# Kernel tuning notes

Measured on AMD Instinct MI355X. Metric: run time of the kernel, lower is better.

The kernel has to match this reference:

```python
import jax, jax.numpy as jnp
import numpy as np

N, E, D = 50000, 800000, 128
SLOPE = 0.2


def setup_inputs() -> dict:
    key = jax.random.key(0)
    ks = jax.random.split(key, 8)
    x = jax.random.normal(ks[0], (N, D), dtype=jnp.float32)
    alpha = jax.random.normal(ks[1], (E, D), dtype=jnp.float32)
    Wl = jax.random.normal(ks[2], (D, D), dtype=jnp.float32) / np.sqrt(D).astype(np.float32)
    bl = jax.random.normal(ks[3], (D,), dtype=jnp.float32) * 0.01
    Wr = jax.random.normal(ks[4], (D, D), dtype=jnp.float32) / np.sqrt(D).astype(np.float32)
    br = jax.random.normal(ks[5], (D,), dtype=jnp.float32) * 0.01
    src = jax.random.randint(ks[6], (E,), 0, N, dtype=jnp.int64)
    dst = jax.random.randint(ks[7], (E,), 0, N, dtype=jnp.int64)
    return {"x": x, "alpha": alpha, "Wl": Wl, "bl": bl, "Wr": Wr, "br": br, "src": src, "dst": dst}


def reference(x, alpha, Wl, bl, Wr, br, src, dst):
    n_nodes = x.shape[0]
    # Dense projections: Mu_l(x), Mu_r(x)  -> [N, D]
    hl = x @ Wl.T + bl
    hr = x @ Wr.T + br
    # Edge-wise score: leakyrelu((h_l[src] + h_r[dst]) * alpha)  -> [E, D]
    s = (jnp.take(hl, src, axis=0) + jnp.take(hr, dst, axis=0)) * alpha
    s = jnp.where(s >= 0, s, SLOPE * s)
    # Edge softmax grouped by destination node (per feature channel), numerically stable
    smax = jax.ops.segment_max(s, dst, num_segments=n_nodes)  # [N, D]
    e = jnp.exp(s - jnp.take(smax, dst, axis=0))
    denom = jax.ops.segment_sum(e, dst, num_segments=n_nodes)  # [N, D]
    att = e / jnp.take(denom, dst, axis=0)
    # Weighted scatter-sum aggregation: sum_{e: dst(e)=v} x[src(e)] * att[e]
    msg = jnp.take(x, src, axis=0) * att  # [E, D]
    return jax.ops.segment_sum(msg, dst, num_segments=n_nodes)  # [N, D]
```

## Files before the change

kernel.cpp:

```cpp
#include <hip/hip_runtime.h>
#include <hip/hip_bf16.h>

#define D 128
#define SLOPE 0.2f
#define CAP 64

typedef float f4 __attribute__((ext_vector_type(4)));
typedef unsigned int v4u __attribute__((ext_vector_type(4)));
typedef unsigned short v4h __attribute__((ext_vector_type(4)));
typedef unsigned int u32;
typedef unsigned short u16;


__global__ void zero_kernel(int* __restrict__ p, int n) {
  int i = blockIdx.x * blockDim.x + threadIdx.x;
  if (i < n) p[i] = 0;
}


__global__ void scatter_bucket(const int* __restrict__ dst, const int* __restrict__ src,
                               int* __restrict__ cnt, long long* __restrict__ eperm, int E) {
  int i = blockIdx.x * blockDim.x + threadIdx.x;
  if (i < E) {
    int d = dst[i];
    int p = atomicAdd(&cnt[d], 1);
    if (p < CAP) {
      long long v = (long long)(unsigned int)i | ((long long)src[i] << 32);
      __builtin_nontemporal_store(v, &eperm[(size_t)d * CAP + p]);
    }
  }
}


__global__ void transpose_w(const float* __restrict__ Wl, const float* __restrict__ Wr,
                            float* __restrict__ wcatT) {
  int i = blockIdx.x * blockDim.x + threadIdx.x;
  int k = i >> 8, c = i & 255;
  float v = (c < D) ? Wl[c * D + k] : Wr[(c - D) * D + k];
  wcatT[k * 256 + c] = v;
}


__device__ __forceinline__ u16 bf16r(float f) {
  u32 u = __float_as_uint(f);
  return (u16)((u + 0x7FFFu + ((u >> 16) & 1u)) >> 16);
}

__global__ __launch_bounds__(256) void gemm_hlr(const float* __restrict__ x,
    const float* __restrict__ wcatT, const float* __restrict__ bl,
    const float* __restrict__ br, u16* __restrict__ hx, float* __restrict__ hr,
    int nrows) {
  __shared__ float xs[64 * 128];
  int t = threadIdx.x;
  int row0 = blockIdx.x << 6;
#pragma unroll
  for (int i = 0; i < 8; ++i) {
    int g = t + (i << 8);
    int r = g >> 5, c4 = (g & 31) << 2;
    int gr = row0 + r;
    float4 v = make_float4(0.f, 0.f, 0.f, 0.f);
    if (gr < nrows) v = *(const float4*)(x + (size_t)gr * D + c4);
    *(float4*)(xs + r * 128 + c4) = v;
  }
  __syncthreads();
  int rg = t >> 5, cg = t & 31;
  int r0 = rg << 3, c0 = cg << 3;
  float acc[8][8];
#pragma unroll
  for (int i = 0; i < 8; ++i)
#pragma unroll
    for (int j = 0; j < 8; ++j) acc[i][j] = 0.f;

  for (int kk = 0; kk < 128; kk += 4) {
    float4 xv[8];
#pragma unroll
    for (int i = 0; i < 8; ++i) xv[i] = *(const float4*)(xs + (r0 + i) * 128 + kk);
#pragma unroll
    for (int dk = 0; dk < 4; ++dk) {
      float4 wa = *(const float4*)(wcatT + (kk + dk) * 256 + c0);
      float4 wb = *(const float4*)(wcatT + (kk + dk) * 256 + c0 + 4);
      float wv0 = wa.x, wv1 = wa.y, wv2 = wa.z, wv3 = wa.w;
      float wv4 = wb.x, wv5 = wb.y, wv6 = wb.z, wv7 = wb.w;
#pragma unroll
      for (int i = 0; i < 8; ++i) {
        float xk = (dk == 0) ? xv[i].x : (dk == 1) ? xv[i].y : (dk == 2) ? xv[i].z : xv[i].w;
        acc[i][0] = fmaf(xk, wv0, acc[i][0]);
        acc[i][1] = fmaf(xk, wv1, acc[i][1]);
        acc[i][2] = fmaf(xk, wv2, acc[i][2]);
        acc[i][3] = fmaf(xk, wv3, acc[i][3]);
        acc[i][4] = fmaf(xk, wv4, acc[i][4]);
        acc[i][5] = fmaf(xk, wv5, acc[i][5]);
        acc[i][6] = fmaf(xk, wv6, acc[i][6]);
        acc[i][7] = fmaf(xk, wv7, acc[i][7]);
      }
    }
  }
  float bias[8];
#pragma unroll
  for (int j = 0; j < 8; ++j) bias[j] = (c0 < D) ? bl[c0 + j] : br[c0 - D + j];
#pragma unroll
  for (int i = 0; i < 8; ++i) {
    int gr = row0 + r0 + i;
    if (gr >= nrows) continue;
    if (c0 < D) {
      v4h a, b2;
#pragma unroll
      for (int j = 0; j < 4; ++j) a[j] = bf16r(acc[i][j] + bias[j]);
#pragma unroll
      for (int j = 0; j < 4; ++j) b2[j] = bf16r(acc[i][4 + j] + bias[4 + j]);
      u16* rowp = hx + (size_t)gr * 256;
      *(v4h*)(rowp + 2 * c0) = a;
      *(v4h*)(rowp + 2 * c0 + 8) = b2;
    } else {
      float* base = hr + (size_t)gr * D + (c0 - D);
      float4 o0 = make_float4(acc[i][0] + bias[0], acc[i][1] + bias[1],
                              acc[i][2] + bias[2], acc[i][3] + bias[3]);
      float4 o1 = make_float4(acc[i][4] + bias[4], acc[i][5] + bias[5],
                              acc[i][6] + bias[6], acc[i][7] + bias[7]);
      *(float4*)(base) = o0;
      *(float4*)(base + 4) = o1;
    }
  }
#pragma unroll
  for (int i = 0; i < 8; ++i) {
    int g = t + (i << 8);
    int r = g >> 5, c4 = (g & 31) << 2;
    int gr = row0 + r;
    if (gr < nrows) {
      const float* sp = xs + r * 128 + c4;
      v4h h;
#pragma unroll
      for (int j = 0; j < 4; ++j) h[j] = bf16r(sp[j]);
      *(v4h*)(hx + (size_t)gr * 256 + 2 * c4 + 4) = h;
    }
  }
}


__device__ __forceinline__ f4 ld4(const float* p) { return *(const f4*)p; }
__device__ __forceinline__ f4 ld4nt(const float* p) {
  return __builtin_nontemporal_load((const f4*)p);
}

__global__ __launch_bounds__(256) void node_attn(const u16* __restrict__ hx,
    const float* __restrict__ alpha, const float* __restrict__ hr,
    const long long* __restrict__ eperm, const int* __restrict__ cnt,
    float* __restrict__ out, int n) {
  int wid = threadIdx.x >> 6, lane = threadIdx.x & 63;
  int v = (blockIdx.x << 2) + wid;
  if (v >= n) return;
  int deg = cnt[v];
  if (deg > CAP) deg = CAP;
  int half = lane >> 5;
  int ch = (lane & 31) << 2;

  if (deg == 0) {
    if (half == 0) {
      f4 z = {0.f, 0.f, 0.f, 0.f};
      *(f4*)(out + (size_t)v * D + ch) = z;
    }
    return;
  }

  const long long* ep = eperm + (size_t)v * CAP;
  f4 hrv = ld4(hr + (size_t)v * D + ch);
  f4 dx = {0.f, 0.f, 0.f, 0.f};
  f4 ox = {0.f, 0.f, 0.f, 0.f};

  int ed[4], ss[4];
  float mk[4];
#define LOADIDX(base, EDA, SSA, MKA)                    \
  {                                                     \
    _Pragma("unroll")                                   \
    for (int u = 0; u < 4; ++u) {                       \
      int idx = (base) + 2 * u + half;                  \
      int j = (idx < deg) ? idx : (deg - 1);            \
      long long pq = ep[j];                             \
      EDA[u] = (int)(unsigned int)pq;                   \
      SSA[u] = (int)(pq >> 32);                         \
      MKA[u] = (idx < deg) ? 1.f : 0.f;                 \
    }                                                   \
  }

  int i = 0;
  LOADIDX(i, ed, ss, mk)
  while (true) {
    f4 av[4];
    v4u gv[4];
#pragma unroll
    for (int u = 0; u < 4; ++u) av[u] = ld4nt(alpha + (size_t)ed[u] * D + ch);
#pragma unroll
    for (int u = 0; u < 4; ++u)
      gv[u] = *(const v4u*)(hx + (size_t)ss[u] * 256 + (ch << 1));

    int inext = i + 8;
    bool more = inext < deg;
    int edn[4], ssn[4];
    float mkn[4];
    if (more) LOADIDX(inext, edn, ssn, mkn)

#pragma unroll
    for (int u = 0; u < 4; ++u) {
      f4 h, xv;
      h[0] = __uint_as_float((gv[u].x & 0xFFFFu) << 16);
      h[1] = __uint_as_float(gv[u].x & 0xFFFF0000u);
      h[2] = __uint_as_float((gv[u].y & 0xFFFFu) << 16);
      h[3] = __uint_as_float(gv[u].y & 0xFFFF0000u);
      xv[0] = __uint_as_float((gv[u].z & 0xFFFFu) << 16);
      xv[1] = __uint_as_float(gv[u].z & 0xFFFF0000u);
      xv[2] = __uint_as_float((gv[u].w & 0xFFFFu) << 16);
      xv[3] = __uint_as_float(gv[u].w & 0xFFFF0000u);
      f4 t = (h + hrv) * av[u];
      f4 ev;
#pragma unroll
      for (int k = 0; k < 4; ++k) {
        float tt = t[k];
        tt = (tt >= 0.f) ? tt : SLOPE * tt;
        ev[k] = __expf(tt);
      }
      ev *= mk[u];
      dx += ev;
      ox += xv * ev;
    }
    if (!more) break;
    i = inext;
#pragma unroll
    for (int u = 0; u < 4; ++u) { ed[u] = edn[u]; ss[u] = ssn[u]; mk[u] = mkn[u]; }
  }
#undef LOADIDX

#pragma unroll
  for (int k = 0; k < 4; ++k) {
    dx[k] += __shfl_xor(dx[k], 32);
    ox[k] += __shfl_xor(ox[k], 32);
  }
  if (half == 0) {
    f4 r;
#pragma unroll
    for (int k = 0; k < 4; ++k) r[k] = ox[k] / dx[k];
    *(f4*)(out + (size_t)v * D + ch) = r;
  }
}

extern "C" void kernel_launch(void* const* d_in, const int* in_sizes, int n_in,
                              void* d_out, int out_size, void* d_ws, size_t ws_size,
                              hipStream_t stream) {
  const float* x = (const float*)d_in[0];
  const float* alpha = (const float*)d_in[1];
  const float* Wl = (const float*)d_in[2];
  const float* bl = (const float*)d_in[3];
  const float* Wr = (const float*)d_in[4];
  const float* br = (const float*)d_in[5];
  const int* src = (const int*)d_in[6];
  const int* dst = (const int*)d_in[7];
  int N = in_sizes[0] / D;
  int E = in_sizes[6];
  float* out = (float*)d_out;

  char* ws = (char*)d_ws;
  auto al = [](size_t v) { return (v + 255) & ~(size_t)255; };
  size_t off = 0;
  u16* hx = (u16*)(ws + off); off += al((size_t)N * 256 * 2);
  float* hr = (float*)(ws + off); off += al((size_t)N * D * 4);
  float* wcatT = (float*)(ws + off); off += al(128 * 256 * 4);
  int* cnt = (int*)(ws + off); off += al((size_t)N * 4);
  long long* eperm = (long long*)(ws + off); off += al((size_t)N * CAP * 8);
  (void)off; (void)ws_size; (void)n_in; (void)out_size;

  const int tb = 256;
  zero_kernel<<<(N + tb - 1) / tb, tb, 0, stream>>>(cnt, N);
  scatter_bucket<<<(E + tb - 1) / tb, tb, 0, stream>>>(dst, src, cnt, eperm, E);
  transpose_w<<<(128 * 256) / tb, tb, 0, stream>>>(Wl, Wr, wcatT);
  gemm_hlr<<<(N + 63) / 64, 256, 0, stream>>>(x, wcatT, bl, br, hx, hr, N);
  node_attn<<<(N + 3) / 4, 256, 0, stream>>>(hx, alpha, hr, eperm, cnt, out, N);
}
```

Measured before the change: 249.5 us.

## Replace FP32 SIMT projection GEMM with bf16 MFMA and pre-converted operands

Adds a pass that converts x to bf16 (also writing the bf16 x half of hx and zeroing counts) and packs the weights into a k-blocked bf16 layout. The scalar-FMA fp32 GEMM is replaced by an MFMA 16x16x32 bf16 kernel where each wave computes 16 rows by 256 columns. The aim is to cut GEMM compute time using matrix cores. In exchange it adds an extra pass over x, lowers projection precision to bf16 inputs, and uses scattered 2-byte output stores.

```diff
diff --git a/kernel.cpp b/kernel.cpp
--- a/kernel.cpp
+++ b/kernel.cpp
@@ -8,13 +8,42 @@
 typedef float f4 __attribute__((ext_vector_type(4)));
 typedef unsigned int v4u __attribute__((ext_vector_type(4)));
 typedef unsigned short v4h __attribute__((ext_vector_type(4)));
+typedef short s8v __attribute__((ext_vector_type(8)));
 typedef unsigned int u32;
 typedef unsigned short u16;
 
-
-__global__ void zero_kernel(int* __restrict__ p, int n) {
+__device__ __forceinline__ u16 bf16r(float f) {
+  u32 u = __float_as_uint(f);
+  return (u16)((u + 0x7FFFu + ((u >> 16) & 1u)) >> 16);
+}
+
+
+__global__ void convert_x(const float* __restrict__ x, u16* __restrict__ xbf,
+                          u16* __restrict__ hx, int* __restrict__ cnt, int N) {
   int i = blockIdx.x * blockDim.x + threadIdx.x;
-  if (i < n) p[i] = 0;
+  if (i < N) cnt[i] = 0;
+  if (i >= N * 16) return;
+  int row = i >> 4, c0 = (i & 15) << 3;
+  const float* xp = x + (size_t)row * D + c0;
+  float4 v0 = *(const float4*)xp;
+  float4 v1 = *(const float4*)(xp + 4);
+  v4h h0, h1;
+  h0[0] = bf16r(v0.x); h0[1] = bf16r(v0.y); h0[2] = bf16r(v0.z); h0[3] = bf16r(v0.w);
+  h1[0] = bf16r(v1.x); h1[1] = bf16r(v1.y); h1[2] = bf16r(v1.z); h1[3] = bf16r(v1.w);
+  *(v4h*)(xbf + (size_t)row * D + c0) = h0;
+  *(v4h*)(xbf + (size_t)row * D + c0 + 4) = h1;
+  u16* hp = hx + (size_t)row * 256;
+  *(v4h*)(hp + 2 * c0 + 4) = h0;
+  *(v4h*)(hp + 2 * c0 + 12) = h1;
+}
+
+
+__global__ void prep_w(const float* __restrict__ Wl, const float* __restrict__ Wr,
+                       u16* __restrict__ wcatB) {
+  int i = blockIdx.x * blockDim.x + threadIdx.x;
+  int k = i >> 8, c = i & 255;
+  float v = (c < D) ? Wl[c * D + k] : Wr[(c - D) * D + k];
+  wcatB[((k >> 3) << 11) + (c << 3) + (k & 7)] = bf16r(v);
 }
 
 
@@ -32,106 +61,53 @@
 }
 
 
-__global__ void transpose_w(const float* __restrict__ Wl, const float* __restrict__ Wr,
-                            float* __restrict__ wcatT) {
-  int i = blockIdx.x * blockDim.x + threadIdx.x;
-  int k = i >> 8, c = i & 255;
-  float v = (c < D) ? Wl[c * D + k] : Wr[(c - D) * D + k];
-  wcatT[k * 256 + c] = v;
-}
-
-
-__device__ __forceinline__ u16 bf16r(float f) {
-  u32 u = __float_as_uint(f);
-  return (u16)((u + 0x7FFFu + ((u >> 16) & 1u)) >> 16);
-}
-
-__global__ __launch_bounds__(256) void gemm_hlr(const float* __restrict__ x,
-    const float* __restrict__ wcatT, const float* __restrict__ bl,
+__global__ __launch_bounds__(256) void gemm_mfma(const u16* __restrict__ xbf,
+    const u16* __restrict__ wcatB, const float* __restrict__ bl,
     const float* __restrict__ br, u16* __restrict__ hx, float* __restrict__ hr,
-    int nrows) {
-  __shared__ float xs[64 * 128];
-  int t = threadIdx.x;
-  int row0 = blockIdx.x << 6;
-#pragma unroll
-  for (int i = 0; i < 8; ++i) {
-    int g = t + (i << 8);
-    int r = g >> 5, c4 = (g & 31) << 2;
-    int gr = row0 + r;
-    float4 v = make_float4(0.f, 0.f, 0.f, 0.f);
-    if (gr < nrows) v = *(const float4*)(x + (size_t)gr * D + c4);
-    *(float4*)(xs + r * 128 + c4) = v;
-  }
-  __syncthreads();
-  int rg = t >> 5, cg = t & 31;
-  int r0 = rg << 3, c0 = cg << 3;
-  float acc[8][8];
-#pragma unroll
-  for (int i = 0; i < 8; ++i)
-#pragma unroll
-    for (int j = 0; j < 8; ++j) acc[i][j] = 0.f;
-
-  for (int kk = 0; kk < 128; kk += 4) {
-    float4 xv[8];
-#pragma unroll
-    for (int i = 0; i < 8; ++i) xv[i] = *(const float4*)(xs + (r0 + i) * 128 + kk);
-#pragma unroll
-    for (int dk = 0; dk < 4; ++dk) {
-      float4 wa = *(const float4*)(wcatT + (kk + dk) * 256 + c0);
-      float4 wb = *(const float4*)(wcatT + (kk + dk) * 256 + c0 + 4);
-      float wv0 = wa.x, wv1 = wa.y, wv2 = wa.z, wv3 = wa.w;
-      float wv4 = wb.x, wv5 = wb.y, wv6 = wb.z, wv7 = wb.w;
-#pragma unroll
-      for (int i = 0; i < 8; ++i) {
-        float xk = (dk == 0) ? xv[i].x : (dk == 1) ? xv[i].y : (dk == 2) ? xv[i].z : xv[i].w;
-        acc[i][0] = fmaf(xk, wv0, acc[i][0]);
-        acc[i][1] = fmaf(xk, wv1, acc[i][1]);
-        acc[i][2] = fmaf(xk, wv2, acc[i][2]);
-        acc[i][3] = fmaf(xk, wv3, acc[i][3]);
-        acc[i][4] = fmaf(xk, wv4, acc[i][4]);
-        acc[i][5] = fmaf(xk, wv5, acc[i][5]);
-        acc[i][6] = fmaf(xk, wv6, acc[i][6]);
-        acc[i][7] = fmaf(xk, wv7, acc[i][7]);
-      }
-    }
-  }
-  float bias[8];
-#pragma unroll
-  for (int j = 0; j < 8; ++j) bias[j] = (c0 < D) ? bl[c0 + j] : br[c0 - D + j];
-#pragma unroll
-  for (int i = 0; i < 8; ++i) {
-    int gr = row0 + r0 + i;
-    if (gr >= nrows) continue;
-    if (c0 < D) {
-      v4h a, b2;
-#pragma unroll
-      for (int j = 0; j < 4; ++j) a[j] = bf16r(acc[i][j] + bias[j]);
-#pragma unroll
-      for (int j = 0; j < 4; ++j) b2[j] = bf16r(acc[i][4 + j] + bias[4 + j]);
-      u16* rowp = hx + (size_t)gr * 256;
-      *(v4h*)(rowp + 2 * c0) = a;
-      *(v4h*)(rowp + 2 * c0 + 8) = b2;
-    } else {
-      float* base = hr + (size_t)gr * D + (c0 - D);
-      float4 o0 = make_float4(acc[i][0] + bias[0], acc[i][1] + bias[1],
-                              acc[i][2] + bias[2], acc[i][3] + bias[3]);
-      float4 o1 = make_float4(acc[i][4] + bias[4], acc[i][5] + bias[5],
-                              acc[i][6] + bias[6], acc[i][7] + bias[7]);
-      *(float4*)(base) = o0;
-      *(float4*)(base + 4) = o1;
-    }
-  }
-#pragma unroll
-  for (int i = 0; i < 8; ++i) {
-    int g = t + (i << 8);
-    int r = g >> 5, c4 = (g & 31) << 2;
-    int gr = row0 + r;
-    if (gr < nrows) {
-      const float* sp = xs + r * 128 + c4;
-      v4h h;
-#pragma unroll
-      for (int j = 0; j < 4; ++j) h[j] = bf16r(sp[j]);
-      *(v4h*)(hx + (size_t)gr * 256 + 2 * c4 + 4) = h;
+    int N) {
+  int w = threadIdx.x >> 6, l = threadIdx.x & 63;
+  int r0 = blockIdx.x * 64 + w * 16;
+  if (r0 >= N) return;
+  int mrow = l & 15, kg = l >> 4;
+  int arow = r0 + mrow;
+  if (arow >= N) arow = N - 1;
+  const u16* xrow = xbf + (size_t)arow * D;
+
+  f4 acc[16];
+#pragma unroll
+  for (int t = 0; t < 16; ++t) acc[t] = (f4){0.f, 0.f, 0.f, 0.f};
+
+#pragma unroll
+  for (int k0 = 0; k0 < 128; k0 += 32) {
+    s8v a = *(const s8v*)(xrow + k0 + (kg << 3));
+    const u16* wb = wcatB + (((k0 >> 3) + kg) << 11) + (mrow << 3);
+#pragma unroll
+    for (int t = 0; t < 16; ++t) {
+      s8v b = *(const s8v*)(wb + t * 128);
+      acc[t] = __builtin_amdgcn_mfma_f32_16x16x32_bf16(a, b, acc[t], 0, 0, 0);
+    }
+  }
+
+  int rbase = r0 + ((l >> 4) << 2);
+#pragma unroll
+  for (int t = 0; t < 8; ++t) {
+    int c = t * 16 + mrow;
+    float bias = bl[c];
+    int slot = ((c >> 2) << 3) + (c & 3);
+#pragma unroll
+    for (int r = 0; r < 4; ++r) {
+      int gr = rbase + r;
+      if (gr < N) hx[(size_t)gr * 256 + slot] = bf16r(acc[t][r] + bias);
+    }
+  }
+#pragma unroll
+  for (int t = 8; t < 16; ++t) {
+    int c = (t - 8) * 16 + mrow;
+    float bias = br[c];
+#pragma unroll
+    for (int r = 0; r < 4; ++r) {
+      int gr = rbase + r;
+      if (gr < N) hr[(size_t)gr * D + c] = acc[t][r] + bias;
     }
   }
 }
@@ -262,15 +238,16 @@
   size_t off = 0;
   u16* hx = (u16*)(ws + off); off += al((size_t)N * 256 * 2);
   float* hr = (float*)(ws + off); off += al((size_t)N * D * 4);
-  float* wcatT = (float*)(ws + off); off += al(128 * 256 * 4);
+  u16* xbf = (u16*)(ws + off); off += al((size_t)N * D * 2);
+  u16* wcatB = (u16*)(ws + off); off += al(128 * 256 * 2);
   int* cnt = (int*)(ws + off); off += al((size_t)N * 4);
   long long* eperm = (long long*)(ws + off); off += al((size_t)N * CAP * 8);
   (void)off; (void)ws_size; (void)n_in; (void)out_size;
 
   const int tb = 256;
-  zero_kernel<<<(N + tb - 1) / tb, tb, 0, stream>>>(cnt, N);
+  convert_x<<<(N * 16 + tb - 1) / tb, tb, 0, stream>>>(x, xbf, hx, cnt, N);
+  prep_w<<<(128 * 256) / tb, tb, 0, stream>>>(Wl, Wr, wcatB);
   scatter_bucket<<<(E + tb - 1) / tb, tb, 0, stream>>>(dst, src, cnt, eperm, E);
-  transpose_w<<<(128 * 256) / tb, tb, 0, stream>>>(Wl, Wr, wcatT);
-  gemm_hlr<<<(N + 63) / 64, 256, 0, stream>>>(x, wcatT, bl, br, hx, hr, N);
+  gemm_mfma<<<(N + 63) / 64, 256, 0, stream>>>(xbf, wcatB, bl, br, hx, hr, N);
   node_attn<<<(N + 3) / 4, 256, 0, stream>>>(hx, alpha, hr, eperm, cnt, out, N);
 }
```

Measured after the change: 221.1 us. 1.13x faster.
